# Performance work log

Hardware: AMD Instinct MI355X
Metric: run time of the kernel (lower is better)

Reference implementation:

```python
import jax, jax.numpy as jnp
import numpy as np

B, T, D, H = 4, 2048, 1024, 16
DH = D // H
T2 = T // 2
LN_EPS = 1e-5


def setup_inputs() -> dict:
    key = jax.random.key(0)
    ks = jax.random.split(key, 10)
    x = jax.random.normal(ks[0], (B, T, D), dtype=jnp.float32)
    query = jax.random.normal(ks[1], (1, 1, D), dtype=jnp.float32) * 0.02
    s = 1.0 / np.sqrt(D)
    Wk = jax.random.uniform(ks[2], (D, D), jnp.float32, -s, s)
    Wv = jax.random.uniform(ks[3], (D, D), jnp.float32, -s, s)
    Wt = jax.random.uniform(ks[4], (D, D // 2), jnp.float32, -s, s)
    bt = jax.random.uniform(ks[5], (D // 2,), jnp.float32, -s, s)
    Wm = jax.random.uniform(ks[6], (D, 1), jnp.float32, -s, s)
    bm = jax.random.uniform(ks[7], (1,), jnp.float32, -s, s)
    ln_g = jnp.ones((D,), jnp.float32)
    ln_b = jnp.zeros((D,), jnp.float32)
    return {"x": x, "query": query, "Wk": Wk, "Wv": Wv, "Wt": Wt,
            "bt": bt, "Wm": Wm, "bm": bm, "ln_g": ln_g, "ln_b": ln_b}


def reference(x, query, Wk, Wv, Wt, bt, Wm, bm, ln_g, ln_b):
    Bx, Tx, d = x.shape
    t2 = Tx // 2
    h, dh = H, DH
    # projections -> (B, T, H, dh)
    k = (x @ Wk).reshape(Bx, Tx, h, dh)
    v = (x @ Wv).reshape(Bx, Tx, h, dh)
    q = query.reshape(h, dh)  # single learned query, shared over all coarse positions
    # scores: (B, H, T) then broadcast to (B, H, T2, T) with position-dependent mask t > 2j
    scores = jnp.einsum('hd,bthd->bht', q, k) / jnp.sqrt(jnp.asarray(dh, x.dtype))
    j_idx = jnp.arange(t2)[:, None]   # (T2, 1)
    t_idx = jnp.arange(Tx)[None, :]   # (1, T)
    mask_bias = jnp.where(t_idx > 2 * j_idx, -jnp.inf, 0.0).astype(x.dtype)  # (T2, T)
    attn = jax.nn.softmax(scores[:, :, None, :] + mask_bias[None, None], axis=-1)  # (B,H,T2,T)
    pooled = jnp.einsum('bhjt,bthd->bjhd', attn, v).reshape(Bx, t2, d)  # (B, T2, d)
    # LayerNorm over last dim
    mu = jnp.mean(pooled, axis=-1, keepdims=True)
    var = jnp.mean(jnp.square(pooled - mu), axis=-1, keepdims=True)
    pooled_n = (pooled - mu) * jax.lax.rsqrt(var + LN_EPS) * ln_g + ln_b
    theta = pooled_n @ Wt + bt                 # (B, T2, d//2)
    mag = jax.nn.sigmoid(pooled_n @ Wm + bm)   # (B, T2, 1)
    return theta, mag
```

## Files before the change

kernel.cpp:

```cpp
#include <hip/hip_runtime.h>
#include <hip/hip_bf16.h>
#include <cstdint>
#include <cstddef>

constexpr int Bc  = 4;
constexpr int Tc  = 2048;
constexpr int Dc  = 1024;
constexpr int Hc  = 16;
constexpr int DHc = 64;
constexpr int T2c = 1024;
constexpr int NCc = 32;
#define LN_EPS_F 1e-5f

typedef __attribute__((ext_vector_type(8))) short bf16x8;
typedef __attribute__((ext_vector_type(8))) ushort ushort8_t;
typedef __attribute__((ext_vector_type(4))) float f32x4;

__device__ inline ushort f2bf(float f) {
    union { float f; uint32_t u; } v; v.f = f;
    uint32_t r = v.u + 0x7FFFu + ((v.u >> 16) & 1u);
    return (ushort)(r >> 16);
}
__device__ inline float bf2f(ushort u) {
    union { uint32_t u; float f; } v; v.u = ((uint32_t)u) << 16;
    return v.f;
}

__device__ inline void store_out(float v, float* p)  { *p = v; }
__device__ inline void store_out(float v, ushort* p) { *p = f2bf(v); }

__device__ inline void async_copy16(const void* g, void* lds) {
    __builtin_amdgcn_global_load_lds(
        (const __attribute__((address_space(1))) void*)g,
        (__attribute__((address_space(3))) void*)lds, 16, 0, 0);
}

__global__ __launch_bounds__(256) void k_cvt(const float* __restrict__ in,
                                             ushort* __restrict__ out, int n) {
    int i = (blockIdx.x * 256 + threadIdx.x) * 4;
    if (i >= n) return;
    float4 f = *(const float4*)(in + i);
    ushort4 o;
    o.x = f2bf(f.x); o.y = f2bf(f.y); o.z = f2bf(f.z); o.w = f2bf(f.w);
    *(ushort4*)(out + i) = o;
}

__global__ __launch_bounds__(256) void k_cvt_t(const float* __restrict__ W,
                                               ushort* __restrict__ Wtp,
                                               int K, int N) {
    __shared__ float tile[32][33];
    int bx = blockIdx.x;
    int by = blockIdx.y;
    int tx = threadIdx.x & 31, ty = threadIdx.x >> 5;
    #pragma unroll
    for (int r = 0; r < 32; r += 8)
        tile[ty + r][tx] = W[(size_t)(by * 32 + ty + r) * N + bx * 32 + tx];
    __syncthreads();
    #pragma unroll
    for (int r = 0; r < 32; r += 8)
        Wtp[(size_t)(bx * 32 + ty + r) * K + by * 32 + tx] = f2bf(tile[tx][ty + r]);
}

__global__ __launch_bounds__(256) void k_qk(const float* __restrict__ Wk,
                                            const float* __restrict__ query,
                                            ushort* __restrict__ qkb) {
    int idx = blockIdx.x * 256 + threadIdx.x;
    if (idx >= Hc * Dc) return;
    int h = idx / Dc, i = idx % Dc;
    const float* wrow = Wk + (size_t)i * Dc + h * DHc;
    const float* qh   = query + h * DHc;
    float s = 0.f;
    #pragma unroll 8
    for (int d = 0; d < DHc; ++d) s += wrow[d] * qh[d];
    qkb[h * Dc + i] = f2bf(s * 0.125f);
}

__global__ __launch_bounds__(64) void k_scores(const ushort* __restrict__ xb,
                                               const ushort* __restrict__ qkb,
                                               float* __restrict__ scores) {
    int lane = threadIdx.x;
    int l15 = lane & 15, quad = lane >> 4;
    int row0 = blockIdx.x * 16;
    f32x4 acc = {};
    const ushort* arow = xb + (size_t)(row0 + l15) * Dc + quad * 8;
    const ushort* brow = qkb + (size_t)l15 * Dc + quad * 8;
    #pragma unroll 8
    for (int k0 = 0; k0 < Dc; k0 += 32) {
        bf16x8 a = *(const bf16x8*)(arow + k0);
        bf16x8 b = *(const bf16x8*)(brow + k0);
        acc = __builtin_amdgcn_mfma_f32_16x16x32_bf16(a, b, acc, 0, 0, 0);
    }
    int b = row0 >> 11;
    int t0 = row0 & (Tc - 1);
    #pragma unroll
    for (int r = 0; r < 4; ++r) {
        int t = t0 + quad * 4 + r;
        scores[((size_t)b * Hc + l15) * Tc + t] = acc[r];
    }
}

template <bool BIAS, typename OutT>
__global__ __launch_bounds__(256) void k_gemm_bf16(const ushort* __restrict__ A,
                                                   const ushort* __restrict__ Bt,
                                                   const float* __restrict__ bias,
                                                   OutT* __restrict__ C,
                                                   int M, int N, int K) {
    __shared__ ushort As[128 * 32];
    __shared__ ushort Bs[128 * 32];
    int tid = threadIdx.x;
    int wid = tid >> 6, lane = tid & 63;
    int tile_m = blockIdx.y * 128, tile_n = blockIdx.x * 128;
    int wm = wid >> 1, wn = wid & 1;

    f32x4 acc[4][4] = {};

    int lrow = lane >> 2;
    int lchunk = lane & 3;
    int quad = lane >> 4, l15 = lane & 15;

    for (int k0 = 0; k0 < K; k0 += 32) {
        #pragma unroll
        for (int r = 0; r < 2; ++r) {
            int rowgrp = wid * 2 + r;
            int row = rowgrp * 16 + lrow;
            const ushort* g = A + (size_t)(tile_m + row) * K + k0 + lchunk * 8;
            async_copy16(g, &As[rowgrp * 16 * 32]);
        }
        #pragma unroll
        for (int r = 0; r < 2; ++r) {
            int rowgrp = wid * 2 + r;
            int row = rowgrp * 16 + lrow;
            const ushort* g = Bt + (size_t)(tile_n + row) * K + k0 + lchunk * 8;
            async_copy16(g, &Bs[rowgrp * 16 * 32]);
        }
        __syncthreads();

        bf16x8 a_frag[4], b_frag[4];
        #pragma unroll
        for (int i = 0; i < 4; ++i)
            a_frag[i] = *(const bf16x8*)&As[(wm * 64 + i * 16 + l15) * 32 + quad * 8];
        #pragma unroll
        for (int j = 0; j < 4; ++j)
            b_frag[j] = *(const bf16x8*)&Bs[(wn * 64 + j * 16 + l15) * 32 + quad * 8];
        #pragma unroll
        for (int i = 0; i < 4; ++i)
            #pragma unroll
            for (int j = 0; j < 4; ++j)
                acc[i][j] = __builtin_amdgcn_mfma_f32_16x16x32_bf16(
                    a_frag[i], b_frag[j], acc[i][j], 0, 0, 0);
        __syncthreads();
    }

    #pragma unroll
    for (int j = 0; j < 4; ++j) {
        int col = tile_n + wn * 64 + j * 16 + l15;
        float bv = BIAS ? bias[col] : 0.f;
        #pragma unroll
        for (int i = 0; i < 4; ++i) {
            #pragma unroll
            for (int r = 0; r < 4; ++r) {
                int row = tile_m + wm * 64 + i * 16 + quad * 4 + r;
                store_out(acc[i][j][r] + bv, &C[(size_t)row * N + col]);
            }
        }
    }
}

__global__ __launch_bounds__(64) void k_chunk(const float* __restrict__ scores,
                                              const ushort* __restrict__ v,
                                              float* __restrict__ chunkL,
                                              float* __restrict__ chunkAcc) {
    int idx = blockIdx.x;
    int c = idx & (NCc - 1);
    int bh = idx / NCc;
    int h = bh & (Hc - 1), b = bh / Hc;
    int lane = threadIdx.x;
    int tgrp = lane >> 3;
    int dgrp = lane & 7;
    int t0 = c * 64;
    const float* srow = scores + (size_t)bh * Tc + t0;
    const ushort* vbase = v + ((size_t)b * Tc + t0) * Dc + h * DHc + dgrp * 8;
    float acc[8] = {};
    float lsum = 0.f;
    #pragma unroll
    for (int it = 0; it < 8; ++it) {
        int t = it * 8 + tgrp;
        float e = expf(srow[t]);
        ushort8_t vv = *(const ushort8_t*)(vbase + (size_t)t * Dc);
        #pragma unroll
        for (int k = 0; k < 8; ++k) acc[k] += e * bf2f(vv[k]);
        lsum += e;
    }
    #pragma unroll
    for (int m = 8; m < 64; m <<= 1) {
        #pragma unroll
        for (int k = 0; k < 8; ++k) acc[k] += __shfl_xor(acc[k], m);
        lsum += __shfl_xor(lsum, m);
    }
    if (tgrp == 0) {
        float4 lo = {acc[0], acc[1], acc[2], acc[3]};
        float4 hi = {acc[4], acc[5], acc[6], acc[7]};
        *(float4*)&chunkAcc[(size_t)idx * DHc + dgrp * 8]     = lo;
        *(float4*)&chunkAcc[(size_t)idx * DHc + dgrp * 8 + 4] = hi;
        if (dgrp == 0) chunkL[idx] = lsum;
    }
}

__global__ __launch_bounds__(64) void k_prefix(const float* __restrict__ chunkL,
                                               const float* __restrict__ chunkAcc,
                                               float* __restrict__ pfxL,
                                               float* __restrict__ pfxAcc) {
    int bh = blockIdx.x;
    int lane = threadIdx.x;
    float accP = 0.f, lP = 0.f;
    for (int c = 0; c < NCc; ++c) {
        size_t idx = (size_t)bh * NCc + c;
        pfxAcc[idx * DHc + lane] = accP;
        if (lane == 0) pfxL[idx] = lP;
        accP += chunkAcc[idx * DHc + lane];
        lP += chunkL[idx];
    }
}

__global__ __launch_bounds__(64) void k_emit(const float* __restrict__ scores,
                                             const ushort* __restrict__ v,
                                             const float* __restrict__ pfxL,
                                             const float* __restrict__ pfxAcc,
                                             ushort* __restrict__ pooled) {
    int idx = blockIdx.x;
    int c = idx & (NCc - 1);
    int bh = idx / NCc;
    int h = bh & (Hc - 1), b = bh / Hc;
    int lane = threadIdx.x;
    int tgrp = lane >> 3, dgrp = lane & 7;
    int t0 = c * 64;
    __shared__ float E[64];
    __shared__ ushort vs[64 * DHc];
    E[lane] = expf(scores[(size_t)bh * Tc + t0 + lane]);
    const ushort* vbase = v + ((size_t)b * Tc + t0) * Dc + h * DHc + dgrp * 8;
    #pragma unroll
    for (int it = 0; it < 8; ++it) {
        int t = it * 8 + tgrp;
        *(ushort8_t*)&vs[t * DHc + dgrp * 8] = *(const ushort8_t*)(vbase + (size_t)t * Dc);
    }
    __syncthreads();
    float acc = pfxAcc[(size_t)idx * DHc + lane];
    float l = pfxL[idx];
    #pragma unroll 4
    for (int t = 0; t < 64; t += 2) {
        float e = E[t];
        acc += e * bf2f(vs[t * DHc + lane]);
        l += e;
        int j = (t0 + t) >> 1;
        pooled[((size_t)b * T2c + j) * Dc + h * DHc + lane] = f2bf(acc / l);
        float e2 = E[t + 1];
        acc += e2 * bf2f(vs[(t + 1) * DHc + lane]);
        l += e2;
    }
}

__global__ __launch_bounds__(256) void k_ln(const ushort* __restrict__ pooled,
                                            const float* __restrict__ g,
                                            const float* __restrict__ be,
                                            ushort* __restrict__ out) {
    int row = blockIdx.x;
    const ushort* p = pooled + (size_t)row * Dc;
    int tid = threadIdx.x;
    __shared__ float red[256];
    __shared__ float mu_s, rstd_s;
    float x4[4];
    {
        ushort4 u = *(const ushort4*)(p + tid * 4);
        x4[0] = bf2f(u.x); x4[1] = bf2f(u.y); x4[2] = bf2f(u.z); x4[3] = bf2f(u.w);
    }
    float s = x4[0] + x4[1] + x4[2] + x4[3];
    red[tid] = s;
    __syncthreads();
    for (int off = 128; off > 0; off >>= 1) {
        if (tid < off) red[tid] += red[tid + off];
        __syncthreads();
    }
    if (tid == 0) mu_s = red[0] * (1.f / Dc);
    __syncthreads();
    float mu = mu_s;
    float vs = 0.f;
    #pragma unroll
    for (int k = 0; k < 4; ++k) { float d = x4[k] - mu; vs += d * d; }
    red[tid] = vs;
    __syncthreads();
    for (int off = 128; off > 0; off >>= 1) {
        if (tid < off) red[tid] += red[tid + off];
        __syncthreads();
    }
    if (tid == 0) rstd_s = rsqrtf(red[0] * (1.f / Dc) + LN_EPS_F);
    __syncthreads();
    float rstd = rstd_s;
    ushort4 o;
    int i = tid * 4;
    o.x = f2bf((x4[0] - mu) * rstd * g[i]     + be[i]);
    o.y = f2bf((x4[1] - mu) * rstd * g[i + 1] + be[i + 1]);
    o.z = f2bf((x4[2] - mu) * rstd * g[i + 2] + be[i + 2]);
    o.w = f2bf((x4[3] - mu) * rstd * g[i + 3] + be[i + 3]);
    *(ushort4*)(out + (size_t)row * Dc + i) = o;
}

__global__ __launch_bounds__(256) void k_mag(const ushort* __restrict__ pn,
                                             const float* __restrict__ Wm,
                                             const float* __restrict__ bm,
                                             float* __restrict__ out) {
    int row = blockIdx.x;
    const ushort* p = pn + (size_t)row * Dc;
    int tid = threadIdx.x;
    float s = 0.f;
    for (int i = tid; i < Dc; i += 256) s += bf2f(p[i]) * Wm[i];
    __shared__ float red[256];
    red[tid] = s;
    __syncthreads();
    for (int off = 128; off > 0; off >>= 1) {
        if (tid < off) red[tid] += red[tid + off];
        __syncthreads();
    }
    if (tid == 0) {
        float z = red[0] + bm[0];
        out[row] = 1.f / (1.f + expf(-z));
    }
}

extern "C" void kernel_launch(void* const* d_in, const int* in_sizes, int n_in,
                              void* d_out, int out_size, void* d_ws, size_t ws_size,
                              hipStream_t stream) {
    const float* x     = (const float*)d_in[0];
    const float* query = (const float*)d_in[1];
    const float* Wk    = (const float*)d_in[2];
    const float* Wv    = (const float*)d_in[3];
    const float* Wt    = (const float*)d_in[4];
    const float* bt    = (const float*)d_in[5];
    const float* Wm    = (const float*)d_in[6];
    const float* bm    = (const float*)d_in[7];
    const float* ln_g  = (const float*)d_in[8];
    const float* ln_b  = (const float*)d_in[9];
    float* out = (float*)d_out;

    char* w = (char*)d_ws;
    auto alloc = [&](size_t bytes) { char* p = w; w += (bytes + 255) & ~(size_t)255; return p; };
    ushort* v        = (ushort*)alloc((size_t)Bc * Tc * Dc * 2);
    ushort* pooled   = (ushort*)alloc((size_t)Bc * T2c * Dc * 2);
    ushort* xb       = (ushort*)alloc((size_t)Bc * Tc * Dc * 2);
    ushort* pooledn  = (ushort*)alloc((size_t)Bc * T2c * Dc * 2);
    ushort* WvT      = (ushort*)alloc((size_t)Dc * Dc * 2);
    ushort* WtT      = (ushort*)alloc((size_t)(Dc / 2) * Dc * 2);
    float*  scores   = (float*) alloc((size_t)Bc * Hc * Tc * 4);
    ushort* qkb      = (ushort*)alloc((size_t)Hc * Dc * 2);
    float*  chunkL   = (float*) alloc((size_t)Bc * Hc * NCc * 4);
    float*  chunkAcc = (float*) alloc((size_t)Bc * Hc * NCc * DHc * 4);
    float*  pfxL     = (float*) alloc((size_t)Bc * Hc * NCc * 4);
    float*  pfxAcc   = (float*) alloc((size_t)Bc * Hc * NCc * DHc * 4);

    k_cvt<<<(Bc * Tc * Dc / 4 + 255) / 256, 256, 0, stream>>>(x, xb, Bc * Tc * Dc);
    k_cvt_t<<<dim3(Dc / 32, Dc / 32), 256, 0, stream>>>(Wv, WvT, Dc, Dc);
    k_cvt_t<<<dim3((Dc / 2) / 32, Dc / 32), 256, 0, stream>>>(Wt, WtT, Dc, Dc / 2);
    k_qk<<<(Hc * Dc + 255) / 256, 256, 0, stream>>>(Wk, query, qkb);
    k_scores<<<(Bc * Tc) / 16, 64, 0, stream>>>(xb, qkb, scores);
    k_gemm_bf16<false, ushort><<<dim3(Dc / 128, (Bc * Tc) / 128), 256, 0, stream>>>(
        xb, WvT, nullptr, v, Bc * Tc, Dc, Dc);
    k_chunk<<<Bc * Hc * NCc, 64, 0, stream>>>(scores, v, chunkL, chunkAcc);
    k_prefix<<<Bc * Hc, 64, 0, stream>>>(chunkL, chunkAcc, pfxL, pfxAcc);
    k_emit<<<Bc * Hc * NCc, 64, 0, stream>>>(scores, v, pfxL, pfxAcc, pooled);
    k_ln<<<Bc * T2c, 256, 0, stream>>>(pooled, ln_g, ln_b, pooledn);
    k_gemm_bf16<true, float><<<dim3((Dc / 2) / 128, (Bc * T2c) / 128), 256, 0, stream>>>(
        pooledn, WtT, bt, out, Bc * T2c, Dc / 2, Dc);
    k_mag<<<Bc * T2c, 256, 0, stream>>>(pooledn, Wm, bm, out + (size_t)Bc * T2c * (Dc / 2));
}
```

Before: 203.3 us.

## Fuse prep kernels, fold scores into V GEMM, inline prefix, fuse LN with mag

```diff
diff --git a/kernel.cpp b/kernel.cpp
--- a/kernel.cpp
+++ b/kernel.cpp
@@ -10,6 +10,7 @@
 constexpr int DHc = 64;
 constexpr int T2c = 1024;
 constexpr int NCc = 32;
+constexpr int NEXT = 1152;
 #define LN_EPS_F 1e-5f
 
 typedef __attribute__((ext_vector_type(8))) short bf16x8;
@@ -35,67 +36,136 @@
         (__attribute__((address_space(3))) void*)lds, 16, 0, 0);
 }
 
-__global__ __launch_bounds__(256) void k_cvt(const float* __restrict__ in,
-                                             ushort* __restrict__ out, int n) {
-    int i = (blockIdx.x * 256 + threadIdx.x) * 4;
-    if (i >= n) return;
-    float4 f = *(const float4*)(in + i);
-    ushort4 o;
-    o.x = f2bf(f.x); o.y = f2bf(f.y); o.z = f2bf(f.z); o.w = f2bf(f.w);
-    *(ushort4*)(out + i) = o;
-}
-
-__global__ __launch_bounds__(256) void k_cvt_t(const float* __restrict__ W,
-                                               ushort* __restrict__ Wtp,
-                                               int K, int N) {
+constexpr int PREP_CVT  = 8192;
+constexpr int PREP_WV   = PREP_CVT + 1024;
+constexpr int PREP_WT   = PREP_WV + 512;
+constexpr int PREP_QK   = PREP_WT + 64;
+constexpr int PREP_ZERO = PREP_QK + 56;
+
+__global__ __launch_bounds__(256) void k_prep(const float* __restrict__ x,
+                                              const float* __restrict__ Wv,
+                                              const float* __restrict__ Wt,
+                                              const float* __restrict__ Wk,
+                                              const float* __restrict__ query,
+                                              ushort* __restrict__ xb,
+                                              ushort* __restrict__ WvXT,
+                                              ushort* __restrict__ WtT) {
     __shared__ float tile[32][33];
-    int bx = blockIdx.x;
-    int by = blockIdx.y;
-    int tx = threadIdx.x & 31, ty = threadIdx.x >> 5;
-    #pragma unroll
-    for (int r = 0; r < 32; r += 8)
-        tile[ty + r][tx] = W[(size_t)(by * 32 + ty + r) * N + bx * 32 + tx];
-    __syncthreads();
-    #pragma unroll
-    for (int r = 0; r < 32; r += 8)
-        Wtp[(size_t)(bx * 32 + ty + r) * K + by * 32 + tx] = f2bf(tile[tx][ty + r]);
-}
-
-__global__ __launch_bounds__(256) void k_qk(const float* __restrict__ Wk,
-                                            const float* __restrict__ query,
-                                            ushort* __restrict__ qkb) {
-    int idx = blockIdx.x * 256 + threadIdx.x;
-    if (idx >= Hc * Dc) return;
-    int h = idx / Dc, i = idx % Dc;
-    const float* wrow = Wk + (size_t)i * Dc + h * DHc;
-    const float* qh   = query + h * DHc;
-    float s = 0.f;
-    #pragma unroll 8
-    for (int d = 0; d < DHc; ++d) s += wrow[d] * qh[d];
-    qkb[h * Dc + i] = f2bf(s * 0.125f);
-}
-
-__global__ __launch_bounds__(64) void k_scores(const ushort* __restrict__ xb,
-                                               const ushort* __restrict__ qkb,
-                                               float* __restrict__ scores) {
-    int lane = threadIdx.x;
-    int l15 = lane & 15, quad = lane >> 4;
-    int row0 = blockIdx.x * 16;
-    f32x4 acc = {};
-    const ushort* arow = xb + (size_t)(row0 + l15) * Dc + quad * 8;
-    const ushort* brow = qkb + (size_t)l15 * Dc + quad * 8;
-    #pragma unroll 8
-    for (int k0 = 0; k0 < Dc; k0 += 32) {
-        bf16x8 a = *(const bf16x8*)(arow + k0);
-        bf16x8 b = *(const bf16x8*)(brow + k0);
-        acc = __builtin_amdgcn_mfma_f32_16x16x32_bf16(a, b, acc, 0, 0, 0);
-    }
-    int b = row0 >> 11;
-    int t0 = row0 & (Tc - 1);
-    #pragma unroll
-    for (int r = 0; r < 4; ++r) {
-        int t = t0 + quad * 4 + r;
-        scores[((size_t)b * Hc + l15) * Tc + t] = acc[r];
+    int blk = blockIdx.x;
+    int tid = threadIdx.x;
+    if (blk < PREP_CVT) {
+        int i = (blk * 256 + tid) * 4;
+        float4 f = *(const float4*)(x + i);
+        ushort4 o;
+        o.x = f2bf(f.x); o.y = f2bf(f.y); o.z = f2bf(f.z); o.w = f2bf(f.w);
+        *(ushort4*)(xb + i) = o;
+    } else if (blk < PREP_WV) {
+        int b2 = blk - PREP_CVT;
+        int bx = b2 & 31, by = b2 >> 5;
+        int tx = tid & 31, ty = tid >> 5;
+        #pragma unroll
+        for (int r = 0; r < 32; r += 8)
+            tile[ty + r][tx] = Wv[(size_t)(by * 32 + ty + r) * Dc + bx * 32 + tx];
+        __syncthreads();
+        #pragma unroll
+        for (int r = 0; r < 32; r += 8)
+            WvXT[(size_t)(bx * 32 + ty + r) * Dc + by * 32 + tx] = f2bf(tile[tx][ty + r]);
+    } else if (blk < PREP_WT) {
+        int b2 = blk - PREP_WV;
+        int bx = b2 & 15, by = b2 >> 4;
+        int tx = tid & 31, ty = tid >> 5;
+        #pragma unroll
+        for (int r = 0; r < 32; r += 8)
+            tile[ty + r][tx] = Wt[(size_t)(by * 32 + ty + r) * (Dc / 2) + bx * 32 + tx];
+        __syncthreads();
+        #pragma unroll
+        for (int r = 0; r < 32; r += 8)
+            WtT[(size_t)(bx * 32 + ty + r) * Dc + by * 32 + tx] = f2bf(tile[tx][ty + r]);
+    } else if (blk < PREP_QK) {
+        int idx = (blk - PREP_WT) * 256 + tid;
+        int h = idx >> 10, i = idx & (Dc - 1);
+        const float* wrow = Wk + (size_t)i * Dc + h * DHc;
+        const float* qh   = query + h * DHc;
+        float s = 0.f;
+        #pragma unroll 8
+        for (int d = 0; d < DHc; ++d) s += wrow[d] * qh[d];
+        WvXT[(size_t)(Dc + h) * Dc + i] = f2bf(s * 0.125f);
+    } else {
+        int idx = (blk - PREP_QK) * 256 + tid;
+        uint4 z = {0, 0, 0, 0};
+        *(uint4*)(WvXT + (size_t)1040 * Dc + idx * 8) = z;
+    }
+}
+
+__global__ __launch_bounds__(256) void k_gemm_v(const ushort* __restrict__ A,
+                                                const ushort* __restrict__ Bt,
+                                                ushort* __restrict__ v,
+                                                float* __restrict__ scores) {
+    constexpr int K = Dc;
+    __shared__ ushort As[128 * 32];
+    __shared__ ushort Bs[128 * 32];
+    int tid = threadIdx.x;
+    int wid = tid >> 6, lane = tid & 63;
+    int tile_m = blockIdx.y * 128, tile_n = blockIdx.x * 128;
+    int wm = wid >> 1, wn = wid & 1;
+
+    f32x4 acc[4][4] = {};
+
+    int lrow = lane >> 2;
+    int lchunk = lane & 3;
+    int quad = lane >> 4, l15 = lane & 15;
+
+    for (int k0 = 0; k0 < K; k0 += 32) {
+        #pragma unroll
+        for (int r = 0; r < 2; ++r) {
+            int rowgrp = wid * 2 + r;
+            int row = rowgrp * 16 + lrow;
+            async_copy16(A + (size_t)(tile_m + row) * K + k0 + lchunk * 8,
+                         &As[rowgrp * 16 * 32]);
+        }
+        #pragma unroll
+        for (int r = 0; r < 2; ++r) {
+            int rowgrp = wid * 2 + r;
+            int row = rowgrp * 16 + lrow;
+            async_copy16(Bt + (size_t)(tile_n + row) * K + k0 + lchunk * 8,
+                         &Bs[rowgrp * 16 * 32]);
+        }
+        __syncthreads();
+
+        bf16x8 a_frag[4], b_frag[4];
+        #pragma unroll
+        for (int i = 0; i < 4; ++i)
+            a_frag[i] = *(const bf16x8*)&As[(wm * 64 + i * 16 + l15) * 32 + quad * 8];
+        #pragma unroll
+        for (int j = 0; j < 4; ++j)
+            b_frag[j] = *(const bf16x8*)&Bs[(wn * 64 + j * 16 + l15) * 32 + quad * 8];
+        #pragma unroll
+        for (int i = 0; i < 4; ++i)
+            #pragma unroll
+            for (int j = 0; j < 4; ++j)
+                acc[i][j] = __builtin_amdgcn_mfma_f32_16x16x32_bf16(
+                    a_frag[i], b_frag[j], acc[i][j], 0, 0, 0);
+        __syncthreads();
+    }
+
+    #pragma unroll
+    for (int j = 0; j < 4; ++j) {
+        int col = tile_n + wn * 64 + j * 16 + l15;
+        #pragma unroll
+        for (int i = 0; i < 4; ++i) {
+            #pragma unroll
+            for (int r = 0; r < 4; ++r) {
+                int row = tile_m + wm * 64 + i * 16 + quad * 4 + r;
+                float val = acc[i][j][r];
+                if (col < Dc) {
+                    v[(size_t)row * Dc + col] = f2bf(val);
+                } else if (col < Dc + Hc) {
+                    int h = col - Dc;
+                    int b = row >> 11, t = row & (Tc - 1);
+                    scores[((size_t)b * Hc + h) * Tc + t] = val;
+                }
+            }
+        }
     }
 }
 
@@ -123,15 +193,15 @@
         for (int r = 0; r < 2; ++r) {
             int rowgrp = wid * 2 + r;
             int row = rowgrp * 16 + lrow;
-            const ushort* g = A + (size_t)(tile_m + row) * K + k0 + lchunk * 8;
-            async_copy16(g, &As[rowgrp * 16 * 32]);
+            async_copy16(A + (size_t)(tile_m + row) * K + k0 + lchunk * 8,
+                         &As[rowgrp * 16 * 32]);
         }
         #pragma unroll
         for (int r = 0; r < 2; ++r) {
             int rowgrp = wid * 2 + r;
             int row = rowgrp * 16 + lrow;
-            const ushort* g = Bt + (size_t)(tile_n + row) * K + k0 + lchunk * 8;
-            async_copy16(g, &Bs[rowgrp * 16 * 32]);
+            async_copy16(Bt + (size_t)(tile_n + row) * K + k0 + lchunk * 8,
+                         &Bs[rowgrp * 16 * 32]);
         }
         __syncthreads();
 
@@ -206,26 +276,10 @@
     }
 }
 
-__global__ __launch_bounds__(64) void k_prefix(const float* __restrict__ chunkL,
-                                               const float* __restrict__ chunkAcc,
-                                               float* __restrict__ pfxL,
-                                               float* __restrict__ pfxAcc) {
-    int bh = blockIdx.x;
-    int lane = threadIdx.x;
-    float accP = 0.f, lP = 0.f;
-    for (int c = 0; c < NCc; ++c) {
-        size_t idx = (size_t)bh * NCc + c;
-        pfxAcc[idx * DHc + lane] = accP;
-        if (lane == 0) pfxL[idx] = lP;
-        accP += chunkAcc[idx * DHc + lane];
-        lP += chunkL[idx];
-    }
-}
-
 __global__ __launch_bounds__(64) void k_emit(const float* __restrict__ scores,
                                              const ushort* __restrict__ v,
-                                             const float* __restrict__ pfxL,
-                                             const float* __restrict__ pfxAcc,
+                                             const float* __restrict__ chunkL,
+                                             const float* __restrict__ chunkAcc,
                                              ushort* __restrict__ pooled) {
     int idx = blockIdx.x;
     int c = idx & (NCc - 1);
@@ -243,9 +297,14 @@
         int t = it * 8 + tgrp;
         *(ushort8_t*)&vs[t * DHc + dgrp * 8] = *(const ushort8_t*)(vbase + (size_t)t * Dc);
     }
-    __syncthreads();
-    float acc = pfxAcc[(size_t)idx * DHc + lane];
-    float l = pfxL[idx];
+    float acc = 0.f;
+    for (int cc = 0; cc < c; ++cc)
+        acc += chunkAcc[((size_t)bh * NCc + cc) * DHc + lane];
+    float lP = (lane < c) ? chunkL[bh * NCc + lane] : 0.f;
+    #pragma unroll
+    for (int m = 1; m < 64; m <<= 1) lP += __shfl_xor(lP, m);
+    float l = lP;
+    __syncthreads();
     #pragma unroll 4
     for (int t = 0; t < 64; t += 2) {
         float e = E[t];
@@ -259,10 +318,13 @@
     }
 }
 
-__global__ __launch_bounds__(256) void k_ln(const ushort* __restrict__ pooled,
-                                            const float* __restrict__ g,
-                                            const float* __restrict__ be,
-                                            ushort* __restrict__ out) {
+__global__ __launch_bounds__(256) void k_lnmag(const ushort* __restrict__ pooled,
+                                               const float* __restrict__ g,
+                                               const float* __restrict__ be,
+                                               const float* __restrict__ Wm,
+                                               const float* __restrict__ bm,
+                                               ushort* __restrict__ out,
+                                               float* __restrict__ mag) {
     int row = blockIdx.x;
     const ushort* p = pooled + (size_t)row * Dc;
     int tid = threadIdx.x;
@@ -273,8 +335,7 @@
         ushort4 u = *(const ushort4*)(p + tid * 4);
         x4[0] = bf2f(u.x); x4[1] = bf2f(u.y); x4[2] = bf2f(u.z); x4[3] = bf2f(u.w);
     }
-    float s = x4[0] + x4[1] + x4[2] + x4[3];
-    red[tid] = s;
+    red[tid] = x4[0] + x4[1] + x4[2] + x4[3];
     __syncthreads();
     for (int off = 128; off > 0; off >>= 1) {
         if (tid < off) red[tid] += red[tid + off];
@@ -295,26 +356,18 @@
     if (tid == 0) rstd_s = rsqrtf(red[0] * (1.f / Dc) + LN_EPS_F);
     __syncthreads();
     float rstd = rstd_s;
+    int i = tid * 4;
+    float4 gv = *(const float4*)(g + i);
+    float4 bv = *(const float4*)(be + i);
+    float4 wv = *(const float4*)(Wm + i);
+    float n0 = (x4[0] - mu) * rstd * gv.x + bv.x;
+    float n1 = (x4[1] - mu) * rstd * gv.y + bv.y;
+    float n2 = (x4[2] - mu) * rstd * gv.z + bv.z;
+    float n3 = (x4[3] - mu) * rstd * gv.w + bv.w;
     ushort4 o;
-    int i = tid * 4;
-    o.x = f2bf((x4[0] - mu) * rstd * g[i]     + be[i]);
-    o.y = f2bf((x4[1] - mu) * rstd * g[i + 1] + be[i + 1]);
-    o.z = f2bf((x4[2] - mu) * rstd * g[i + 2] + be[i + 2]);
-    o.w = f2bf((x4[3] - mu) * rstd * g[i + 3] + be[i + 3]);
+    o.x = f2bf(n0); o.y = f2bf(n1); o.z = f2bf(n2); o.w = f2bf(n3);
     *(ushort4*)(out + (size_t)row * Dc + i) = o;
-}
-
-__global__ __launch_bounds__(256) void k_mag(const ushort* __restrict__ pn,
-                                             const float* __restrict__ Wm,
-                                             const float* __restrict__ bm,
-                                             float* __restrict__ out) {
-    int row = blockIdx.x;
-    const ushort* p = pn + (size_t)row * Dc;
-    int tid = threadIdx.x;
-    float s = 0.f;
-    for (int i = tid; i < Dc; i += 256) s += bf2f(p[i]) * Wm[i];
-    __shared__ float red[256];
-    red[tid] = s;
+    red[tid] = bf2f(o.x) * wv.x + bf2f(o.y) * wv.y + bf2f(o.z) * wv.z + bf2f(o.w) * wv.w;
     __syncthreads();
     for (int off = 128; off > 0; off >>= 1) {
         if (tid < off) red[tid] += red[tid + off];
@@ -322,7 +375,7 @@
     }
     if (tid == 0) {
         float z = red[0] + bm[0];
-        out[row] = 1.f / (1.f + expf(-z));
+        mag[row] = 1.f / (1.f + expf(-z));
     }
 }
 
@@ -347,27 +400,18 @@
     ushort* pooled   = (ushort*)alloc((size_t)Bc * T2c * Dc * 2);
     ushort* xb       = (ushort*)alloc((size_t)Bc * Tc * Dc * 2);
     ushort* pooledn  = (ushort*)alloc((size_t)Bc * T2c * Dc * 2);
-    ushort* WvT      = (ushort*)alloc((size_t)Dc * Dc * 2);
+    ushort* WvXT     = (ushort*)alloc((size_t)NEXT * Dc * 2);
     ushort* WtT      = (ushort*)alloc((size_t)(Dc / 2) * Dc * 2);
     float*  scores   = (float*) alloc((size_t)Bc * Hc * Tc * 4);
-    ushort* qkb      = (ushort*)alloc((size_t)Hc * Dc * 2);
     float*  chunkL   = (float*) alloc((size_t)Bc * Hc * NCc * 4);
     float*  chunkAcc = (float*) alloc((size_t)Bc * Hc * NCc * DHc * 4);
-    float*  pfxL     = (float*) alloc((size_t)Bc * Hc * NCc * 4);
-    float*  pfxAcc   = (float*) alloc((size_t)Bc * Hc * NCc * DHc * 4);
-
-    k_cvt<<<(Bc * Tc * Dc / 4 + 255) / 256, 256, 0, stream>>>(x, xb, Bc * Tc * Dc);
-    k_cvt_t<<<dim3(Dc / 32, Dc / 32), 256, 0, stream>>>(Wv, WvT, Dc, Dc);
-    k_cvt_t<<<dim3((Dc / 2) / 32, Dc / 32), 256, 0, stream>>>(Wt, WtT, Dc, Dc / 2);
-    k_qk<<<(Hc * Dc + 255) / 256, 256, 0, stream>>>(Wk, query, qkb);
-    k_scores<<<(Bc * Tc) / 16, 64, 0, stream>>>(xb, qkb, scores);
-    k_gemm_bf16<false, ushort><<<dim3(Dc / 128, (Bc * Tc) / 128), 256, 0, stream>>>(
-        xb, WvT, nullptr, v, Bc * Tc, Dc, Dc);
+
+    k_prep<<<PREP_ZERO, 256, 0, stream>>>(x, Wv, Wt, Wk, query, xb, WvXT, WtT);
+    k_gemm_v<<<dim3(NEXT / 128, (Bc * Tc) / 128), 256, 0, stream>>>(xb, WvXT, v, scores);
     k_chunk<<<Bc * Hc * NCc, 64, 0, stream>>>(scores, v, chunkL, chunkAcc);
-    k_prefix<<<Bc * Hc, 64, 0, stream>>>(chunkL, chunkAcc, pfxL, pfxAcc);
-    k_emit<<<Bc * Hc * NCc, 64, 0, stream>>>(scores, v, pfxL, pfxAcc, pooled);
-    k_ln<<<Bc * T2c, 256, 0, stream>>>(pooled, ln_g, ln_b, pooledn);
+    k_emit<<<Bc * Hc * NCc, 64, 0, stream>>>(scores, v, chunkL, chunkAcc, pooled);
+    k_lnmag<<<Bc * T2c, 256, 0, stream>>>(pooled, ln_g, ln_b, Wm, bm, pooledn,
+                                          out + (size_t)Bc * T2c * (Dc / 2));
     k_gemm_bf16<true, float><<<dim3((Dc / 2) / 128, (Bc * T2c) / 128), 256, 0, stream>>>(
         pooledn, WtT, bt, out, Bc * T2c, Dc / 2, Dc);
-    k_mag<<<Bc * T2c, 256, 0, stream>>>(pooledn, Wm, bm, out + (size_t)Bc * T2c * (Dc / 2));
-}
+}
```

After: 208.2 us. +2.4%, slower.
